# Kernel tuning notes

Hardware: AMD Instinct MI355X
Metric: run time of the kernel (lower is better)

Reference implementation:

```python
import jax, jax.numpy as jnp
import numpy as np

E = 1024   # embed_dim
H = 16     # num_heads
D = E // H # head_dim = 64
HD2 = D // 2
B = 2
S = 2048


def setup_inputs() -> dict:
    key = jax.random.key(0)
    ks = jax.random.split(key, 12)
    def lin(k, fan_in, fan_out):
        # xavier-uniform-ish init, stored in [in, out] (jax) convention
        lim = float(np.sqrt(6.0 / (fan_in + fan_out)))
        return jax.random.uniform(k, (fan_in, fan_out), jnp.float32, -lim, lim)
    return {
        "query": jax.random.normal(ks[0], (B, S, E), jnp.float32),
        "xi_scale": jax.random.uniform(ks[1], (B,), jnp.float32),
        "Wq": lin(ks[2], E, E), "bq": jnp.zeros((E,), jnp.float32),
        "Wk": lin(ks[3], E, E), "bk": jnp.zeros((E,), jnp.float32),
        "Wv": lin(ks[4], E, E), "bv": jnp.zeros((E,), jnp.float32),
        "Wo": lin(ks[5], E, E), "bo": jnp.zeros((E,), jnp.float32),
        "enc_w1": lin(ks[6], 1, HD2), "enc_b1": jnp.zeros((HD2,), jnp.float32),
        "ln_g": jnp.ones((HD2,), jnp.float32), "ln_b": jnp.zeros((HD2,), jnp.float32),
        "enc_w2": lin(ks[7], HD2, D), "enc_b2": jnp.zeros((D,), jnp.float32),
        "scale_gating": jnp.ones((H,), jnp.float32),
    }


def reference(query, xi_scale, Wq, bq, Wk, bk, Wv, bv, Wo, bo,
              enc_w1, enc_b1, ln_g, ln_b, enc_w2, enc_b2, scale_gating):
    b, s, e = query.shape
    h, d = H, e // H
    # --- scale adaptation: xi -> Linear -> LayerNorm -> GELU -> Linear ---
    x = xi_scale[:, None] @ enc_w1 + enc_b1                  # [B, D/2]
    mu = x.mean(-1, keepdims=True)
    var = ((x - mu) ** 2).mean(-1, keepdims=True)
    x = (x - mu) / jnp.sqrt(var + 1e-5) * ln_g + ln_b
    x = jax.nn.gelu(x, approximate=False)
    xe = x @ enc_w2 + enc_b2                                 # [B, D]
    adapt = 1.0 + jax.nn.sigmoid(scale_gating)[None, :, None] * xe[:, None, :]  # [B, H, D]
    # --- projections (self-attention: key = value = query) ---
    q = (query @ Wq + bq).reshape(b, s, h, d).transpose(0, 2, 1, 3) * adapt[:, :, None, :]
    k = (query @ Wk + bk).reshape(b, s, h, d).transpose(0, 2, 1, 3) * adapt[:, :, None, :]
    v = (query @ Wv + bv).reshape(b, s, h, d).transpose(0, 2, 1, 3)
    # --- explicit QK^T / sqrt(d) -> softmax -> V ---
    inv_scale = 1.0 / float(np.sqrt(d))
    scores = jnp.einsum('bhqd,bhkd->bhqk', q, k) * inv_scale  # [B, H, S, S]
    attn = jax.nn.softmax(scores, axis=-1)
    out = jnp.einsum('bhqk,bhkd->bhqd', attn, v)              # [B, H, S, D]
    out = out.transpose(0, 2, 1, 3).reshape(b, s, e)
    return out @ Wo + bo
```

## Files before the change

### kernel.cpp

```cpp
#include <hip/hip_runtime.h>

typedef __bf16 bf16;
typedef __attribute__((ext_vector_type(8))) __bf16 bf16x8;
typedef __attribute__((ext_vector_type(4))) float f32x4;
typedef __attribute__((ext_vector_type(16))) float f32x16;
typedef unsigned int u32;

#define MFMA16(a, b, c) __builtin_amdgcn_mfma_f32_16x16x32_bf16((a), (b), (c), 0, 0, 0)
#define MFMA32(a, b, c) __builtin_amdgcn_mfma_f32_32x32x16_bf16((a), (b), (c), 0, 0, 0)

#define BB 2
#define SS 2048
#define EE 1024
#define HH 16
#define DD 64
#define MM (BB * SS)

#define TM 128
#define TN 64
#define BK 64

__device__ inline f32x4 zero4() {
    f32x4 z; z.x = 0.f; z.y = 0.f; z.z = 0.f; z.w = 0.f; return z;
}

__device__ __forceinline__ void gload16(const bf16* g, bf16* l) {
    __builtin_amdgcn_global_load_lds(
        (const __attribute__((address_space(1))) u32*)(const void*)g,
        (__attribute__((address_space(3))) u32*)(void*)l,
        16, 0, 0);
}

__device__ __forceinline__ u32 pkbf(float a, float b) {
    union { __bf16 h; unsigned short s; } ua, ub;
    ua.h = (__bf16)a; ub.h = (__bf16)b;
    return (u32)ua.s | ((u32)ub.s << 16);
}

__global__ __launch_bounds__(256) void prep_kernel(
    const float* __restrict__ query, bf16* __restrict__ qc,
    const float* __restrict__ s0, const float* __restrict__ s1,
    const float* __restrict__ s2, const float* __restrict__ s3,
    bf16* __restrict__ d0, bf16* __restrict__ d1,
    bf16* __restrict__ d2, bf16* __restrict__ d3,
    const float* __restrict__ xi, const float* __restrict__ w1,
    const float* __restrict__ b1, const float* __restrict__ lng,
    const float* __restrict__ lnb, const float* __restrict__ w2,
    const float* __restrict__ b2, const float* __restrict__ gate,
    float* __restrict__ adapt) {
    __shared__ bf16 tile[64 * 72];
    const int bid = blockIdx.x;
    const int t = threadIdx.x;

    if (bid < 2048) {
        const int i = (bid * 256 + t) * 8;
        float4 a = *(const float4*)(query + i);
        float4 b = *(const float4*)(query + i + 4);
        bf16 tmp[8];
        tmp[0] = (bf16)a.x; tmp[1] = (bf16)a.y; tmp[2] = (bf16)a.z; tmp[3] = (bf16)a.w;
        tmp[4] = (bf16)b.x; tmp[5] = (bf16)b.y; tmp[6] = (bf16)b.z; tmp[7] = (bf16)b.w;
        *(uint4*)(qc + i) = *(uint4*)tmp;
    } else if (bid < 3072) {
        const int m = (bid - 2048) >> 8;
        const int idx0 = (bid - 2048) & 255;
        const float* W = (m == 0) ? s0 : (m == 1) ? s1 : (m == 2) ? s2 : s3;
        bf16* Wt = (m == 0) ? d0 : (m == 1) ? d1 : (m == 2) ? d2 : d3;
        const int k0 = (idx0 >> 4) * 64, n0 = (idx0 & 15) * 64;
#pragma unroll
        for (int i = 0; i < 2; ++i) {
            int idx = i * 256 + t;
            int r = idx >> 3, c = (idx & 7) * 8;
            float4 a = *(const float4*)(W + (k0 + r) * EE + n0 + c);
            float4 b = *(const float4*)(W + (k0 + r) * EE + n0 + c + 4);
            bf16 tmp[8];
            tmp[0] = (bf16)a.x; tmp[1] = (bf16)a.y; tmp[2] = (bf16)a.z; tmp[3] = (bf16)a.w;
            tmp[4] = (bf16)b.x; tmp[5] = (bf16)b.y; tmp[6] = (bf16)b.z; tmp[7] = (bf16)b.w;
            *(uint4*)(tile + r * 72 + c) = *(uint4*)tmp;
        }
        __syncthreads();
#pragma unroll
        for (int i = 0; i < 2; ++i) {
            int idx = i * 256 + t;
            int n = idx >> 3, kc = (idx & 7) * 8;
            bf16 tmp[8];
#pragma unroll
            for (int j = 0; j < 8; ++j) tmp[j] = tile[(kc + j) * 72 + n];
            *(uint4*)(Wt + (n0 + n) * EE + k0 + kc) = *(uint4*)tmp;
        }
    } else {
        const int b = bid - 3072;
        float* xs = (float*)tile;
        if (t < 64) {
            const float xiv = xi[b];
            float xv = 0.f;
            if (t < 32) xv = xiv * w1[t] + b1[t];
            float sm = xv;
            for (int off = 1; off < 32; off <<= 1) sm += __shfl_xor(sm, off);
            const float mu = sm * (1.f / 32.f);
            float dv = (t < 32) ? (xv - mu) : 0.f;
            float s2 = dv * dv;
            for (int off = 1; off < 32; off <<= 1) s2 += __shfl_xor(s2, off);
            const float var = s2 * (1.f / 32.f);
            if (t < 32) {
                float xn = (xv - mu) * rsqrtf(var + 1e-5f) * lng[t] + lnb[t];
                float ge = 0.5f * xn * (1.f + erff(xn * 0.70710678118654752f));
                xs[t] = ge;
            }
        }
        __syncthreads();
        if (t < 64) {
            float acc = b2[t];
            for (int j = 0; j < 32; ++j) acc += xs[j] * w2[j * DD + t];
            for (int h = 0; h < HH; ++h) {
                float sg = 1.f / (1.f + __expf(-gate[h]));
                adapt[(b * HH + h) * DD + t] = 1.f + sg * acc;
            }
        }
    }
}

__global__ __launch_bounds__(256, 3) void gemm_epi(
    const bf16* __restrict__ Aq, const bf16* __restrict__ Bqk,
    const bf16* __restrict__ Av,
    const float* __restrict__ bias, const float* __restrict__ bias2,
    const float* __restrict__ bias3, const float* __restrict__ adapt,
    bf16* __restrict__ outqk, bf16* __restrict__ outvt,
    float* __restrict__ outf, int mode) {
    __shared__ bf16 As[2 * TM * BK];
    __shared__ bf16 Bs[2 * TN * BK];

    const int t = threadIdx.x;
    const int w = t >> 6, lane = t & 63;
    const int mrow = lane & 15, quad = lane >> 4;

    int md = mode, bx, by;
    const bf16 *Ap, *Bp;
    if (mode == 6) {
        int bid = blockIdx.x;
        if (bid < 1024) { md = 5; bx = bid & 31; by = bid >> 5; Ap = Aq; Bp = Bqk; }
        else { md = 4; bid -= 1024; bx = bid & 7; by = bid >> 3; Ap = Av; Bp = Aq; }
    } else {
        bx = blockIdx.x; by = blockIdx.y; Ap = Aq; Bp = Bqk;
    }
    const int m0 = bx * TM, n0 = by * TN;

    f32x4 acc[2][4];
#pragma unroll
    for (int i = 0; i < 2; ++i)
#pragma unroll
        for (int j = 0; j < 4; ++j) acc[i][j] = zero4();

    const int grow = lane >> 3;
    const int gsw = ((lane & 7) ^ grow) * 8;
    const bf16* Ag = Ap + (size_t)(m0 + w * 32 + grow) * EE + gsw;
    const bf16* Bg = Bp + (size_t)(n0 + w * 16 + grow) * EE + gsw;
    bf16* Al = As + (w * 32) * BK;
    bf16* Bl = Bs + (w * 16) * BK;

#pragma unroll
    for (int i = 0; i < 4; ++i) gload16(Ag + i * 8 * EE, Al + i * 8 * BK);
#pragma unroll
    for (int i = 0; i < 2; ++i) gload16(Bg + i * 8 * EE, Bl + i * 8 * BK);

    for (int kt = 0; kt < EE / BK; ++kt) {
        __syncthreads();
        if (kt < EE / BK - 1) {
            const int kn = (kt + 1) * BK;
            const int nb = (kt + 1) & 1;
#pragma unroll
            for (int i = 0; i < 4; ++i)
                gload16(Ag + i * 8 * EE + kn, Al + nb * TM * BK + i * 8 * BK);
#pragma unroll
            for (int i = 0; i < 2; ++i)
                gload16(Bg + i * 8 * EE + kn, Bl + nb * TN * BK + i * 8 * BK);
        }
        const bf16* Ab = As + (kt & 1) * TM * BK;
        const bf16* Bb = Bs + (kt & 1) * TN * BK;
#pragma unroll
        for (int ks = 0; ks < 2; ++ks) {
            const int cg = ks * 4 + quad;
            const int sw = (cg ^ (mrow & 7)) * 8;
            bf16x8 af[2], bfr[4];
#pragma unroll
            for (int mi = 0; mi < 2; ++mi)
                af[mi] = *(const bf16x8*)(Ab + (w * 32 + mi * 16 + mrow) * BK + sw);
#pragma unroll
            for (int nj = 0; nj < 4; ++nj)
                bfr[nj] = *(const bf16x8*)(Bb + (nj * 16 + mrow) * BK + sw);
#pragma unroll
            for (int mi = 0; mi < 2; ++mi)
#pragma unroll
                for (int nj = 0; nj < 4; ++nj)
                    acc[mi][nj] = MFMA16(af[mi], bfr[nj], acc[mi][nj]);
        }
    }

#pragma unroll
    for (int mi = 0; mi < 2; ++mi) {
#pragma unroll
        for (int nj = 0; nj < 4; ++nj) {
            const int col = n0 + nj * 16 + mrow;
#pragma unroll
            for (int r = 0; r < 4; ++r) {
                const int row = m0 + w * 32 + mi * 16 + quad * 4 + r;
                float v = acc[mi][nj][r];
                if (md == 3) {
                    outf[row * EE + col] = v + bias[col];
                } else if (md == 4) {
                    v += bias3[row];
                    const int h = row >> 6, d = row & 63;
                    const int b = col >> 11, s = col & (SS - 1);
                    outvt[(((b * HH + h) * DD + d) * SS) + s] = (bf16)v;
                } else {
                    const int m2 = col >> 10;
                    const int cl = col & 1023;
                    const int h = cl >> 6, d = cl & 63;
                    const int b = row >> 11, s = row & (SS - 1);
                    v += (m2 ? bias2[cl] : bias[cl]);
                    v *= adapt[(b * HH + h) * DD + d];
                    if (!m2) v *= 0.125f;
                    outqk[(size_t)m2 * MM * EE + ((b * HH + h) * SS + s) * DD + d] = (bf16)v;
                }
            }
        }
    }
}

__global__ __launch_bounds__(256, 3) void attn_kernel(
    const bf16* __restrict__ q, const bf16* __restrict__ k,
    const bf16* __restrict__ vt, bf16* __restrict__ o0, bf16* __restrict__ o1,
    float* __restrict__ lws) {
    __shared__ bf16 lds[16384];
    bf16* Ks = lds;
    bf16* Vs = lds + 8192;

    const int t = threadIdx.x;
    const int w = t >> 6, lane = t & 63;
    const int q32 = lane & 31, h = lane >> 5;
    const int split = blockIdx.x >> 9;
    const int rest = blockIdx.x & 511;
    const int bh = rest >> 4;
    const int qb = rest & 15;
    const int qr0 = qb * 128 + w * 32;

    bf16x8 qf[4];
#pragma unroll
    for (int c = 0; c < 4; ++c)
        qf[c] = *(const bf16x8*)(q + (size_t)(bh * SS + qr0 + q32) * DD + c * 16 + h * 8);

    f32x16 oacc[2];
#pragma unroll
    for (int mf = 0; mf < 2; ++mf)
#pragma unroll
        for (int i = 0; i < 16; ++i) oacc[mf][i] = 0.f;
    float lsum = 0.f;

    const int dr = lane >> 3;
    const int dcg = ((lane & 7) ^ dr) * 8;
    const bf16* kg = k + (size_t)bh * SS * DD;
    const bf16* vg = vt + (size_t)bh * DD * SS;
    const bf16* kgl = kg + (size_t)dr * DD + dcg;
    const bf16* vgl = vg + (size_t)(w * 16 + dr) * SS + dcg;

    const int ktbeg = split * (SS / 128), ktend = ktbeg + (SS / 128);

#pragma unroll
    for (int i = 0; i < 2; ++i) {
        const int rb = w * 16 + i * 8;
        gload16(kgl + (size_t)(ktbeg * 64 + rb) * DD, Ks + rb * 64);
        gload16(vgl + (size_t)(i * 8) * SS + ktbeg * 64, Vs + rb * 64);
    }

    for (int kt = ktbeg; kt < ktend; ++kt) {
        __syncthreads();
        if (kt < ktend - 1) {
            const int nb = (kt + 1) & 1;
#pragma unroll
            for (int i = 0; i < 2; ++i) {
                const int rb = w * 16 + i * 8;
                gload16(kgl + (size_t)((kt + 1) * 64 + rb) * DD, Ks + nb * 4096 + rb * 64);
                gload16(vgl + (size_t)(i * 8) * SS + (kt + 1) * 64, Vs + nb * 4096 + rb * 64);
            }
        }
        const bf16* Kb = Ks + (kt & 1) * 4096;
        const bf16* Vb = Vs + (kt & 1) * 4096;

        f32x16 st[2];
#pragma unroll
        for (int mf = 0; mf < 2; ++mf)
#pragma unroll
            for (int i = 0; i < 16; ++i) st[mf][i] = 0.f;
#pragma unroll
        for (int c = 0; c < 4; ++c) {
            const int sw = ((2 * c + h) ^ (q32 & 7)) * 8;
#pragma unroll
            for (int mf = 0; mf < 2; ++mf) {
                bf16x8 kf = *(const bf16x8*)(Kb + (mf * 32 + q32) * 64 + sw);
                st[mf] = MFMA32(kf, qf[c], st[mf]);
            }
        }

        u32 P32[2][8];
#pragma unroll
        for (int mf = 0; mf < 2; ++mf)
#pragma unroll
            for (int rp = 0; rp < 8; ++rp) {
                float pa = __expf(st[mf][2 * rp]);
                float pb = __expf(st[mf][2 * rp + 1]);
                lsum += pa + pb;
                P32[mf][rp] = pkbf(pa, pb);
            }

#pragma unroll
        for (int c = 0; c < 4; ++c) {
            const int mfs = c >> 1;
            const int ro = (c & 1) * 4;
            u32 vA0 = P32[mfs][ro + 0], vA1 = P32[mfs][ro + 1];
            u32 vB0 = P32[mfs][ro + 2], vB1 = P32[mfs][ro + 3];
            u32 prep0 = h ? vA0 : vB0;
            u32 prep1 = h ? vA1 : vB1;
            u32 sh0 = __shfl_xor(prep0, 32);
            u32 sh1 = __shfl_xor(prep1, 32);
            union { u32 u[4]; bf16x8 v; } pb;
            pb.u[0] = h ? sh0 : vA0;
            pb.u[1] = h ? sh1 : vA1;
            pb.u[2] = h ? vB0 : sh0;
            pb.u[3] = h ? vB1 : sh1;
            const int sw = ((2 * c + h) ^ (q32 & 7)) * 8;
#pragma unroll
            for (int mf = 0; mf < 2; ++mf) {
                bf16x8 vf = *(const bf16x8*)(Vb + (mf * 32 + q32) * 64 + sw);
                oacc[mf] = MFMA32(vf, pb.v, oacc[mf]);
            }
        }
    }

    lsum += __shfl_xor(lsum, 32);

    __syncthreads();
    bf16* ob = lds + w * 2112;
#pragma unroll
    for (int mf = 0; mf < 2; ++mf)
#pragma unroll
        for (int rp = 0; rp < 8; ++rp) {
            const int d = 32 * mf + 2 * (rp & 1) + 8 * (rp >> 1) + 4 * h;
            *(u32*)(ob + q32 * 66 + d) = pkbf(oacc[mf][2 * rp], oacc[mf][2 * rp + 1]);
        }
    __builtin_amdgcn_s_waitcnt(0);

    bf16* op = split ? o1 : o0;
    const int b = bh >> 4, head = bh & 15;
    const int qq = lane >> 1, half = lane & 1;
#pragma unroll
    for (int i = 0; i < 4; ++i) {
        bf16x8 val = *(const bf16x8*)(ob + qq * 66 + half * 32 + i * 8);
        *(bf16x8*)(op + (size_t)(b * SS + qr0 + qq) * EE + head * DD +
                   half * 32 + i * 8) = val;
    }
    if (lane < 32)
        lws[split * (32 * SS) + bh * SS + qr0 + q32] = lsum;
}

__global__ __launch_bounds__(256) void combine_kernel(
    const bf16* __restrict__ p1, const float* __restrict__ lws,
    bf16* __restrict__ o) {
    const int i = (blockIdx.x * 256 + threadIdx.x) * 8;
    const int b = i >> 21, s = (i >> 10) & (SS - 1), h = (i >> 6) & 15;
    const int li = (b * HH + h) * SS + s;
    const float inv = 1.f / (lws[li] + lws[32 * SS + li]);
    uint4 u0 = *(const uint4*)(o + i);
    uint4 u1 = *(const uint4*)(p1 + i);
    bf16 a0[8], a1[8], res[8];
    *(uint4*)a0 = u0; *(uint4*)a1 = u1;
#pragma unroll
    for (int j = 0; j < 8; ++j) res[j] = (bf16)(((float)a0[j] + (float)a1[j]) * inv);
    *(uint4*)(o + i) = *(uint4*)res;
}

extern "C" void kernel_launch(void* const* d_in, const int* in_sizes, int n_in,
                              void* d_out, int out_size, void* d_ws, size_t ws_size,
                              hipStream_t stream) {
    const float* query = (const float*)d_in[0];
    const float* xi    = (const float*)d_in[1];
    const float* Wq = (const float*)d_in[2];  const float* bq = (const float*)d_in[3];
    const float* Wk = (const float*)d_in[4];  const float* bk = (const float*)d_in[5];
    const float* Wv = (const float*)d_in[6];  const float* bv = (const float*)d_in[7];
    const float* Wo = (const float*)d_in[8];  const float* bo = (const float*)d_in[9];
    const float* ew1 = (const float*)d_in[10]; const float* eb1 = (const float*)d_in[11];
    const float* lng = (const float*)d_in[12]; const float* lnb = (const float*)d_in[13];
    const float* ew2 = (const float*)d_in[14]; const float* eb2 = (const float*)d_in[15];
    const float* gate = (const float*)d_in[16];
    float* out = (float*)d_out;

    char* ws = (char*)d_ws;
    const size_t SZ = (size_t)MM * EE * sizeof(bf16);
    bf16* queryc = (bf16*)(ws);
    bf16* p0     = (bf16*)(ws);
    bf16* qws    = (bf16*)(ws + SZ);
    bf16* kws    = (bf16*)(ws + 2 * SZ);
    bf16* wqT    = (bf16*)(ws + 3 * SZ);
    bf16* wkT    = (bf16*)(ws + 3 * SZ + 2097152);
    bf16* wvT    = (bf16*)(ws + 3 * SZ + 2 * 2097152);
    bf16* woT    = (bf16*)(ws + 3 * SZ + 3 * 2097152);
    float* adaptws = (float*)(ws + 4 * SZ);
    float* lws   = (float*)(ws + 4 * SZ + 8192);
    bf16* vtws   = (bf16*)d_out;
    bf16* p1     = (bf16*)((char*)d_out + SZ);

    prep_kernel<<<3074, 256, 0, stream>>>(query, queryc, Wq, Wk, Wv, Wo,
                                          wqT, wkT, wvT, woT,
                                          xi, ew1, eb1, lng, lnb, ew2, eb2, gate,
                                          adaptws);

    gemm_epi<<<1536, 256, 0, stream>>>(queryc, wqT, wvT, bq, bk, bv, adaptws,
                                       qws, vtws, nullptr, 6);

    attn_kernel<<<2 * BB * HH * (SS / 128), 256, 0, stream>>>(qws, kws, vtws, p0, p1, lws);
    combine_kernel<<<MM * EE / (256 * 8), 256, 0, stream>>>(p1, lws, p0);

    gemm_epi<<<dim3(MM / TM, EE / TN), 256, 0, stream>>>(
        p0, woT, nullptr, bo, nullptr, nullptr, nullptr, nullptr, nullptr, out, 3);
}
```

Before: 230.9 us.

## Enlarge QKV GEMM tiles to 128x128 and process 64 query rows per attention wave

The QKV projection GEMM becomes its own kernel with 128x128 output tiles, a 2x2 wave layout, and a K-step of 32. This gives more MFMA work per LDS fragment load and halves the block count. The attention kernel now has each wave handle two 32-row query groups against the same K/V fragments, so each LDS read of K and V is reused twice, with occupancy lowered to 2 blocks per SM. The output GEMM is split into a dedicated kernel with the old tiling. In exchange, register pressure rises in both kernels and there are fewer blocks to fill the GPU.

```diff
diff --git a/kernel.cpp b/kernel.cpp
--- a/kernel.cpp
+++ b/kernel.cpp
@@ -15,10 +15,6 @@
 #define HH 16
 #define DD 64
 #define MM (BB * SS)
-
-#define TM 128
-#define TN 64
-#define BK 64
 
 __device__ inline f32x4 zero4() {
     f32x4 z; z.x = 0.f; z.y = 0.f; z.z = 0.f; z.w = 0.f; return z;
@@ -119,94 +115,82 @@
     }
 }
 
-__global__ __launch_bounds__(256, 3) void gemm_epi(
+__global__ __launch_bounds__(256, 3) void gemm_qkv(
     const bf16* __restrict__ Aq, const bf16* __restrict__ Bqk,
     const bf16* __restrict__ Av,
     const float* __restrict__ bias, const float* __restrict__ bias2,
     const float* __restrict__ bias3, const float* __restrict__ adapt,
-    bf16* __restrict__ outqk, bf16* __restrict__ outvt,
-    float* __restrict__ outf, int mode) {
-    __shared__ bf16 As[2 * TM * BK];
-    __shared__ bf16 Bs[2 * TN * BK];
+    bf16* __restrict__ outqk, bf16* __restrict__ outvt) {
+    __shared__ bf16 As[2 * 128 * 32];
+    __shared__ bf16 Bs[2 * 128 * 32];
 
     const int t = threadIdx.x;
     const int w = t >> 6, lane = t & 63;
     const int mrow = lane & 15, quad = lane >> 4;
-
-    int md = mode, bx, by;
+    const int wm = (w & 1) * 64, wn = (w >> 1) * 64;
+
+    int md, bx, by;
     const bf16 *Ap, *Bp;
-    if (mode == 6) {
-        int bid = blockIdx.x;
-        if (bid < 1024) { md = 5; bx = bid & 31; by = bid >> 5; Ap = Aq; Bp = Bqk; }
-        else { md = 4; bid -= 1024; bx = bid & 7; by = bid >> 3; Ap = Av; Bp = Aq; }
-    } else {
-        bx = blockIdx.x; by = blockIdx.y; Ap = Aq; Bp = Bqk;
-    }
-    const int m0 = bx * TM, n0 = by * TN;
-
-    f32x4 acc[2][4];
-#pragma unroll
-    for (int i = 0; i < 2; ++i)
+    int bid = blockIdx.x;
+    if (bid < 512) { md = 5; bx = bid & 31; by = bid >> 5; Ap = Aq; Bp = Bqk; }
+    else { md = 4; bid -= 512; bx = bid & 7; by = bid >> 3; Ap = Av; Bp = Aq; }
+    const int m0 = bx * 128, n0 = by * 128;
+
+    f32x4 acc[4][4];
+#pragma unroll
+    for (int i = 0; i < 4; ++i)
 #pragma unroll
         for (int j = 0; j < 4; ++j) acc[i][j] = zero4();
 
-    const int grow = lane >> 3;
-    const int gsw = ((lane & 7) ^ grow) * 8;
-    const bf16* Ag = Ap + (size_t)(m0 + w * 32 + grow) * EE + gsw;
-    const bf16* Bg = Bp + (size_t)(n0 + w * 16 + grow) * EE + gsw;
-    bf16* Al = As + (w * 32) * BK;
-    bf16* Bl = Bs + (w * 16) * BK;
-
-#pragma unroll
-    for (int i = 0; i < 4; ++i) gload16(Ag + i * 8 * EE, Al + i * 8 * BK);
-#pragma unroll
-    for (int i = 0; i < 2; ++i) gload16(Bg + i * 8 * EE, Bl + i * 8 * BK);
-
-    for (int kt = 0; kt < EE / BK; ++kt) {
+    const int dr = lane >> 2;
+    const int dcg = ((lane & 3) ^ (dr & 3)) * 8;
+    const bf16* Ag = Ap + (size_t)(m0 + w * 16 + dr) * EE + dcg;
+    const bf16* Bg = Bp + (size_t)(n0 + w * 16 + dr) * EE + dcg;
+    bf16* Al = As + (w * 16) * 32;
+    bf16* Bl = Bs + (w * 16) * 32;
+
+    gload16(Ag, Al);
+    gload16(Ag + 64 * EE, Al + 64 * 32);
+    gload16(Bg, Bl);
+    gload16(Bg + 64 * EE, Bl + 64 * 32);
+
+    for (int kt = 0; kt < 32; ++kt) {
         __syncthreads();
-        if (kt < EE / BK - 1) {
-            const int kn = (kt + 1) * BK;
+        if (kt < 31) {
+            const int kn = (kt + 1) * 32;
             const int nb = (kt + 1) & 1;
-#pragma unroll
-            for (int i = 0; i < 4; ++i)
-                gload16(Ag + i * 8 * EE + kn, Al + nb * TM * BK + i * 8 * BK);
-#pragma unroll
-            for (int i = 0; i < 2; ++i)
-                gload16(Bg + i * 8 * EE + kn, Bl + nb * TN * BK + i * 8 * BK);
-        }
-        const bf16* Ab = As + (kt & 1) * TM * BK;
-        const bf16* Bb = Bs + (kt & 1) * TN * BK;
-#pragma unroll
-        for (int ks = 0; ks < 2; ++ks) {
-            const int cg = ks * 4 + quad;
-            const int sw = (cg ^ (mrow & 7)) * 8;
-            bf16x8 af[2], bfr[4];
-#pragma unroll
-            for (int mi = 0; mi < 2; ++mi)
-                af[mi] = *(const bf16x8*)(Ab + (w * 32 + mi * 16 + mrow) * BK + sw);
-#pragma unroll
-            for (int nj = 0; nj < 4; ++nj)
-                bfr[nj] = *(const bf16x8*)(Bb + (nj * 16 + mrow) * BK + sw);
-#pragma unroll
-            for (int mi = 0; mi < 2; ++mi)
-#pragma unroll
-                for (int nj = 0; nj < 4; ++nj)
-                    acc[mi][nj] = MFMA16(af[mi], bfr[nj], acc[mi][nj]);
-        }
-    }
-
-#pragma unroll
-    for (int mi = 0; mi < 2; ++mi) {
-#pragma unroll
-        for (int nj = 0; nj < 4; ++nj) {
-            const int col = n0 + nj * 16 + mrow;
+            gload16(Ag + kn, Al + nb * 4096);
+            gload16(Ag + 64 * EE + kn, Al + nb * 4096 + 64 * 32);
+            gload16(Bg + kn, Bl + nb * 4096);
+            gload16(Bg + 64 * EE + kn, Bl + nb * 4096 + 64 * 32);
+        }
+        const bf16* Ab = As + (kt & 1) * 4096;
+        const bf16* Bb = Bs + (kt & 1) * 4096;
+        const int sw = (quad ^ (mrow & 3)) * 8;
+        bf16x8 af[4], bfr[4];
+#pragma unroll
+        for (int i = 0; i < 4; ++i)
+            af[i] = *(const bf16x8*)(Ab + (wm + i * 16 + mrow) * 32 + sw);
+#pragma unroll
+        for (int j = 0; j < 4; ++j)
+            bfr[j] = *(const bf16x8*)(Bb + (wn + j * 16 + mrow) * 32 + sw);
+#pragma unroll
+        for (int i = 0; i < 4; ++i)
+#pragma unroll
+            for (int j = 0; j < 4; ++j)
+                acc[i][j] = MFMA16(af[i], bfr[j], acc[i][j]);
+    }
+
+#pragma unroll
+    for (int i = 0; i < 4; ++i) {
+#pragma unroll
+        for (int j = 0; j < 4; ++j) {
+            const int col = n0 + wn + j * 16 + mrow;
 #pragma unroll
             for (int r = 0; r < 4; ++r) {
-                const int row = m0 + w * 32 + mi * 16 + quad * 4 + r;
-                float v = acc[mi][nj][r];
-                if (md == 3) {
-                    outf[row * EE + col] = v + bias[col];
-                } else if (md == 4) {
+                const int row = m0 + wm + i * 16 + quad * 4 + r;
+                float v = acc[i][j][r];
+                if (md == 4) {
                     v += bias3[row];
                     const int h = row >> 6, d = row & 63;
                     const int b = col >> 11, s = col & (SS - 1);
@@ -226,34 +210,115 @@
     }
 }
 
-__global__ __launch_bounds__(256, 3) void attn_kernel(
+__global__ __launch_bounds__(256, 3) void gemm_o(
+    const bf16* __restrict__ A, const bf16* __restrict__ Bt,
+    const float* __restrict__ bias, float* __restrict__ outf) {
+    __shared__ bf16 As[2 * 128 * 64];
+    __shared__ bf16 Bs[2 * 64 * 64];
+
+    const int t = threadIdx.x;
+    const int w = t >> 6, lane = t & 63;
+    const int mrow = lane & 15, quad = lane >> 4;
+    const int m0 = blockIdx.x * 128, n0 = blockIdx.y * 64;
+
+    f32x4 acc[2][4];
+#pragma unroll
+    for (int i = 0; i < 2; ++i)
+#pragma unroll
+        for (int j = 0; j < 4; ++j) acc[i][j] = zero4();
+
+    const int grow = lane >> 3;
+    const int gsw = ((lane & 7) ^ grow) * 8;
+    const bf16* Ag = A + (size_t)(m0 + w * 32 + grow) * EE + gsw;
+    const bf16* Bg = Bt + (size_t)(n0 + w * 16 + grow) * EE + gsw;
+    bf16* Al = As + (w * 32) * 64;
+    bf16* Bl = Bs + (w * 16) * 64;
+
+#pragma unroll
+    for (int i = 0; i < 4; ++i) gload16(Ag + i * 8 * EE, Al + i * 8 * 64);
+#pragma unroll
+    for (int i = 0; i < 2; ++i) gload16(Bg + i * 8 * EE, Bl + i * 8 * 64);
+
+    for (int kt = 0; kt < 16; ++kt) {
+        __syncthreads();
+        if (kt < 15) {
+            const int kn = (kt + 1) * 64;
+            const int nb = (kt + 1) & 1;
+#pragma unroll
+            for (int i = 0; i < 4; ++i)
+                gload16(Ag + i * 8 * EE + kn, Al + nb * 8192 + i * 8 * 64);
+#pragma unroll
+            for (int i = 0; i < 2; ++i)
+                gload16(Bg + i * 8 * EE + kn, Bl + nb * 4096 + i * 8 * 64);
+        }
+        const bf16* Ab = As + (kt & 1) * 8192;
+        const bf16* Bb = Bs + (kt & 1) * 4096;
+#pragma unroll
+        for (int ks = 0; ks < 2; ++ks) {
+            const int cg = ks * 4 + quad;
+            const int sw = (cg ^ (mrow & 7)) * 8;
+            bf16x8 af[2], bfr[4];
+#pragma unroll
+            for (int mi = 0; mi < 2; ++mi)
+                af[mi] = *(const bf16x8*)(Ab + (w * 32 + mi * 16 + mrow) * 64 + sw);
+#pragma unroll
+            for (int nj = 0; nj < 4; ++nj)
+                bfr[nj] = *(const bf16x8*)(Bb + (nj * 16 + mrow) * 64 + sw);
+#pragma unroll
+            for (int mi = 0; mi < 2; ++mi)
+#pragma unroll
+                for (int nj = 0; nj < 4; ++nj)
+                    acc[mi][nj] = MFMA16(af[mi], bfr[nj], acc[mi][nj]);
+        }
+    }
+
+#pragma unroll
+    for (int mi = 0; mi < 2; ++mi) {
+#pragma unroll
+        for (int nj = 0; nj < 4; ++nj) {
+            const int col = n0 + nj * 16 + mrow;
+#pragma unroll
+            for (int r = 0; r < 4; ++r) {
+                const int row = m0 + w * 32 + mi * 16 + quad * 4 + r;
+                outf[row * EE + col] = acc[mi][nj][r] + bias[col];
+            }
+        }
+    }
+}
+
+__global__ __launch_bounds__(256, 2) void attn_kernel(
     const bf16* __restrict__ q, const bf16* __restrict__ k,
     const bf16* __restrict__ vt, bf16* __restrict__ o0, bf16* __restrict__ o1,
     float* __restrict__ lws) {
-    __shared__ bf16 lds[16384];
+    __shared__ bf16 lds[16896];
     bf16* Ks = lds;
     bf16* Vs = lds + 8192;
 
     const int t = threadIdx.x;
     const int w = t >> 6, lane = t & 63;
     const int q32 = lane & 31, h = lane >> 5;
-    const int split = blockIdx.x >> 9;
-    const int rest = blockIdx.x & 511;
-    const int bh = rest >> 4;
-    const int qb = rest & 15;
-    const int qr0 = qb * 128 + w * 32;
-
-    bf16x8 qf[4];
-#pragma unroll
-    for (int c = 0; c < 4; ++c)
-        qf[c] = *(const bf16x8*)(q + (size_t)(bh * SS + qr0 + q32) * DD + c * 16 + h * 8);
-
-    f32x16 oacc[2];
-#pragma unroll
-    for (int mf = 0; mf < 2; ++mf)
-#pragma unroll
-        for (int i = 0; i < 16; ++i) oacc[mf][i] = 0.f;
-    float lsum = 0.f;
+    const int split = blockIdx.x >> 8;
+    const int rest = blockIdx.x & 255;
+    const int bh = rest >> 3;
+    const int qb = rest & 7;
+    const int qr0 = qb * 256 + w * 64;
+
+    bf16x8 qf[2][4];
+#pragma unroll
+    for (int qi = 0; qi < 2; ++qi)
+#pragma unroll
+        for (int c = 0; c < 4; ++c)
+            qf[qi][c] = *(const bf16x8*)(q + (size_t)(bh * SS + qr0 + qi * 32 + q32) * DD +
+                                         c * 16 + h * 8);
+
+    f32x16 oacc[2][2];
+#pragma unroll
+    for (int qi = 0; qi < 2; ++qi)
+#pragma unroll
+        for (int mf = 0; mf < 2; ++mf)
+#pragma unroll
+            for (int i = 0; i < 16; ++i) oacc[qi][mf][i] = 0.f;
+    float lsum[2] = {0.f, 0.f};
 
     const int dr = lane >> 3;
     const int dcg = ((lane & 7) ^ dr) * 8;
@@ -285,80 +350,102 @@
         const bf16* Kb = Ks + (kt & 1) * 4096;
         const bf16* Vb = Vs + (kt & 1) * 4096;
 
-        f32x16 st[2];
-#pragma unroll
-        for (int mf = 0; mf < 2; ++mf)
-#pragma unroll
-            for (int i = 0; i < 16; ++i) st[mf][i] = 0.f;
+        f32x16 st[2][2];
+#pragma unroll
+        for (int qi = 0; qi < 2; ++qi)
+#pragma unroll
+            for (int mf = 0; mf < 2; ++mf)
+#pragma unroll
+                for (int i = 0; i < 16; ++i) st[qi][mf][i] = 0.f;
 #pragma unroll
         for (int c = 0; c < 4; ++c) {
             const int sw = ((2 * c + h) ^ (q32 & 7)) * 8;
 #pragma unroll
             for (int mf = 0; mf < 2; ++mf) {
                 bf16x8 kf = *(const bf16x8*)(Kb + (mf * 32 + q32) * 64 + sw);
-                st[mf] = MFMA32(kf, qf[c], st[mf]);
-            }
-        }
-
-        u32 P32[2][8];
-#pragma unroll
-        for (int mf = 0; mf < 2; ++mf)
-#pragma unroll
-            for (int rp = 0; rp < 8; ++rp) {
-                float pa = __expf(st[mf][2 * rp]);
-                float pb = __expf(st[mf][2 * rp + 1]);
-                lsum += pa + pb;
-                P32[mf][rp] = pkbf(pa, pb);
-            }
+#pragma unroll
+                for (int qi = 0; qi < 2; ++qi)
+                    st[qi][mf] = MFMA32(kf, qf[qi][c], st[qi][mf]);
+            }
+        }
+
+        u32 P32[2][2][8];
+#pragma unroll
+        for (int qi = 0; qi < 2; ++qi)
+#pragma unroll
+            for (int mf = 0; mf < 2; ++mf)
+#pragma unroll
+                for (int rp = 0; rp < 8; ++rp) {
+                    float pa = __expf(st[qi][mf][2 * rp]);
+                    float pb = __expf(st[qi][mf][2 * rp + 1]);
+                    lsum[qi] += pa + pb;
+                    P32[qi][mf][rp] = pkbf(pa, pb);
+                }
 
 #pragma unroll
         for (int c = 0; c < 4; ++c) {
             const int mfs = c >> 1;
             const int ro = (c & 1) * 4;
-            u32 vA0 = P32[mfs][ro + 0], vA1 = P32[mfs][ro + 1];
-            u32 vB0 = P32[mfs][ro + 2], vB1 = P32[mfs][ro + 3];
-            u32 prep0 = h ? vA0 : vB0;
-            u32 prep1 = h ? vA1 : vB1;
-            u32 sh0 = __shfl_xor(prep0, 32);
-            u32 sh1 = __shfl_xor(prep1, 32);
-            union { u32 u[4]; bf16x8 v; } pb;
-            pb.u[0] = h ? sh0 : vA0;
-            pb.u[1] = h ? sh1 : vA1;
-            pb.u[2] = h ? vB0 : sh0;
-            pb.u[3] = h ? vB1 : sh1;
+            union { u32 u[4]; bf16x8 v; } pb[2];
+#pragma unroll
+            for (int qi = 0; qi < 2; ++qi) {
+                u32 vA0 = P32[qi][mfs][ro + 0], vA1 = P32[qi][mfs][ro + 1];
+                u32 vB0 = P32[qi][mfs][ro + 2], vB1 = P32[qi][mfs][ro + 3];
+                u32 prep0 = h ? vA0 : vB0;
+                u32 prep1 = h ? vA1 : vB1;
+                u32 sh0 = __shfl_xor(prep0, 32);
+                u32 sh1 = __shfl_xor(prep1, 32);
+                pb[qi].u[0] = h ? sh0 : vA0;
+                pb[qi].u[1] = h ? sh1 : vA1;
+                pb[qi].u[2] = h ? vB0 : sh0;
+                pb[qi].u[3] = h ? vB1 : sh1;
+            }
             const int sw = ((2 * c + h) ^ (q32 & 7)) * 8;
 #pragma unroll
             for (int mf = 0; mf < 2; ++mf) {
                 bf16x8 vf = *(const bf16x8*)(Vb + (mf * 32 + q32) * 64 + sw);
-                oacc[mf] = MFMA32(vf, pb.v, oacc[mf]);
-            }
-        }
-    }
-
-    lsum += __shfl_xor(lsum, 32);
+#pragma unroll
+                for (int qi = 0; qi < 2; ++qi)
+                    oacc[qi][mf] = MFMA32(vf, pb[qi].v, oacc[qi][mf]);
+            }
+        }
+    }
+
+    lsum[0] += __shfl_xor(lsum[0], 32);
+    lsum[1] += __shfl_xor(lsum[1], 32);
 
     __syncthreads();
-    bf16* ob = lds + w * 2112;
-#pragma unroll
-    for (int mf = 0; mf < 2; ++mf)
-#pragma unroll
-        for (int rp = 0; rp < 8; ++rp) {
-            const int d = 32 * mf + 2 * (rp & 1) + 8 * (rp >> 1) + 4 * h;
-            *(u32*)(ob + q32 * 66 + d) = pkbf(oacc[mf][2 * rp], oacc[mf][2 * rp + 1]);
-        }
+    bf16* ob = lds + w * 4224;
+#pragma unroll
+    for (int qi = 0; qi < 2; ++qi)
+#pragma unroll
+        for (int mf = 0; mf < 2; ++mf)
+#pragma unroll
+            for (int rp = 0; rp < 8; ++rp) {
+                const int d = 32 * mf + 2 * (rp & 1) + 8 * (rp >> 1) + 4 * h;
+                *(u32*)(ob + (qi * 32 + q32) * 66 + d) =
+                    pkbf(oacc[qi][mf][2 * rp], oacc[qi][mf][2 * rp + 1]);
+            }
     __builtin_amdgcn_s_waitcnt(0);
 
     bf16* op = split ? o1 : o0;
     const int b = bh >> 4, head = bh & 15;
-    const int qq = lane >> 1, half = lane & 1;
-#pragma unroll
-    for (int i = 0; i < 4; ++i) {
-        bf16x8 val = *(const bf16x8*)(ob + qq * 66 + half * 32 + i * 8);
-        *(bf16x8*)(op + (size_t)(b * SS + qr0 + qq) * EE + head * DD +
-                   half * 32 + i * 8) = val;
-    }
-    if (lane < 32)
-        lws[split * (32 * SS) + bh * SS + qr0 + q32] = lsum;
+    const int half = lane & 1;
+#pragma unroll
+    for (int p = 0; p < 2; ++p) {
+        const int r = p * 32 + (lane >> 1);
+#pragma unroll
+        for (int i = 0; i < 4; ++i) {
+            bf16x8 val = *(const bf16x8*)(ob + r * 66 + half * 32 + i * 8);
+            *(bf16x8*)(op + (size_t)(b * SS + qr0 + r) * EE + head * DD +
+                       half * 32 + i * 8) = val;
+        }
+    }
+    if (lane < 32) {
+#pragma unroll
+        for (int qi = 0; qi < 2; ++qi)
+            lws[split * (32 * SS) + bh * SS + qr0 + qi * 32 + q32] = lsum[qi];
+    }
 }
 
 __global__ __launch_bounds__(256) void combine_kernel(
@@ -412,12 +499,11 @@
                                           xi, ew1, eb1, lng, lnb, ew2, eb2, gate,
                                           adaptws);
 
-    gemm_epi<<<1536, 256, 0, stream>>>(queryc, wqT, wvT, bq, bk, bv, adaptws,
-                                       qws, vtws, nullptr, 6);
-
-    attn_kernel<<<2 * BB * HH * (SS / 128), 256, 0, stream>>>(qws, kws, vtws, p0, p1, lws);
+    gemm_qkv<<<768, 256, 0, stream>>>(queryc, wqT, wvT, bq, bk, bv, adaptws,
+                                      qws, vtws);
+
+    attn_kernel<<<2 * BB * HH * (SS / 256), 256, 0, stream>>>(qws, kws, vtws, p0, p1, lws);
     combine_kernel<<<MM * EE / (256 * 8), 256, 0, stream>>>(p1, lws, p0);
 
-    gemm_epi<<<dim3(MM / TM, EE / TN), 256, 0, stream>>>(
-        p0, woT, nullptr, bo, nullptr, nullptr, nullptr, nullptr, nullptr, out, 3);
-}
+    gemm_o<<<dim3(MM / 128, EE / 64), 256, 0, stream>>>(p0, woT, bo, out);
+}
```

New measurement: 224.2 us. -2.9%, faster.
